# Kernel optimization log

Measured on AMD Instinct MI355X. Metric: run time of the kernel, lower is better.

The kernel has to match this reference:

```python
import jax, jax.numpy as jnp
import numpy as np

DIM = 33  # hardcoded in the torch module


def setup_inputs() -> dict:
    key = jax.random.key(0)
    k1, k2, k3 = jax.random.split(key, 3)
    B, H, W = 8, 512, 512
    inp = jax.random.uniform(k1, (B, 3, H, W), dtype=jnp.float32)
    out = jax.random.uniform(k2, (B, 3, H, W), dtype=jnp.float32)
    mask = (jax.random.uniform(k3, (B, 1, H, W)) > 0.5).astype(jnp.float32)
    return {"mask": mask, "input": inp, "output": out}


def _tridistribute(mask, inp, out, dim=DIM):
    # Trilinear scatter-accumulate of `out` pixel colors into a per-image
    # 3D LUT indexed by `inp` pixel colors, masked, then count-normalized.
    B = inp.shape[0]
    binsize = 1.000001 / (dim - 1)
    x = inp / binsize                              # [B,3,H,W]
    idx = jnp.floor(x).astype(jnp.int32)           # lower bin ids, in [0, dim-2]
    frac = x - jnp.floor(x)                        # trilinear fractions
    r_id, g_id, b_id = idx[:, 0], idx[:, 1], idx[:, 2]
    rd = frac[:, 0].reshape(B, -1)                 # [B,N], N = H*W
    gd = frac[:, 1].reshape(B, -1)
    bd = frac[:, 2].reshape(B, -1)
    base = (r_id + g_id * dim + b_id * dim * dim).reshape(B, -1)  # flat corner 000
    m = (mask[:, 0] > 0).astype(inp.dtype).reshape(B, -1)
    ws, offs = [], []
    for db in (0, 1):
        for dg in (0, 1):
            for dr in (0, 1):
                w = ((rd if dr else 1 - rd) * (gd if dg else 1 - gd) * (bd if db else 1 - bd))
                ws.append(w * m)
                offs.append(dr + dg * dim + db * dim * dim)
    w_all = jnp.stack(ws, 0)                                        # [8,B,N]
    idx_all = base[None] + jnp.asarray(offs, jnp.int32)[:, None, None]  # [8,B,N]
    idx_flat = idx_all.transpose(1, 0, 2).reshape(B, -1)            # [B,8N]
    w_flat = w_all.transpose(1, 0, 2).reshape(B, -1)                # [B,8N]
    out_f = out.reshape(B, 3, -1)                                   # [B,3,N]
    vals = (w_all[:, :, None, :] * out_f[None]).transpose(1, 2, 0, 3).reshape(B, 3, -1)  # [B,3,8N]
    nbins = dim ** 3
    # scatter-add per batch element (vmap over B, then over 3 channels)
    lut = jax.vmap(lambda i, v: jax.vmap(lambda vc: jnp.zeros(nbins, inp.dtype).at[i].add(vc))(v))(idx_flat, vals)  # [B,3,nbins]
    cnt1 = jax.vmap(lambda i, w: jnp.zeros(nbins, inp.dtype).at[i].add(w))(idx_flat, w_flat)  # [B,nbins]
    cnt = jnp.broadcast_to(cnt1[:, None, :], lut.shape)             # same count for all 3 channels
    denom = jnp.where(cnt > 0, cnt, 1.0)
    lut = jnp.where(cnt > 0, lut / denom, 0.0)                      # tridistribute.divide
    shape5 = (B, 3, dim, dim, dim)
    return lut.reshape(shape5), cnt.reshape(shape5)


def reference(mask, input, output):
    lut, lut_count = _tridistribute(mask, input, output)
    return lut, lut_count, output
```

## Files before the change

kernel.cpp:

```cpp
#include <hip/hip_runtime.h>
#include <hip/hip_fp16.h>

#define DIM   33
#define NB    (DIM * DIM * DIM)
#define BATCH 8
#define HW    (512 * 512)
#define SLICE (DIM * DIM)
#define NK1   32
#define CAP1  4416
#define W1    256
#define SPAN1 1024
#define SUB2  4
#define NKEY  1024
#define CAP2  192
#define MAXC2 1120

#define G1_OFF 0
#define G2_OFF 256
#define NCNT   (G2_OFF + BATCH * NKEY)
#define A1     8448
#define S1     (BATCH * NK1 * CAP1)
#define A2     (A1 + 3 * S1)
#define S2     (BATCH * NKEY * CAP2)
#define WS_WORDS (A2 + 3 * S2)

static __device__ __forceinline__ unsigned f2h(float x) {
    return (unsigned)__half_as_ushort(__float2half(x));
}
static __device__ __forceinline__ float h2f(unsigned u) {
    return __half2float(__ushort_as_half((unsigned short)(u & 0xffffu)));
}
static __device__ __forceinline__ unsigned pack2(float a, float b) {
    return f2h(a) | (f2h(b) << 16);
}

__global__ __launch_bounds__(256) void zero_counters(int* __restrict__ ws)
{
    int i = blockIdx.x * 256 + threadIdx.x;
    if (i < NCNT) ws[i] = 0;
}

__global__ __launch_bounds__(256) void sort1(const float* __restrict__ mask,
                                             const float* __restrict__ inp,
                                             const float* __restrict__ outp,
                                             int* __restrict__ ws,
                                             float* __restrict__ outcopy)
{
    __shared__ int hist[NK1], basev[NK1], startL[NK1];
    __shared__ unsigned       stX[SPAN1];
    __shared__ unsigned       stY[SPAN1];
    __shared__ unsigned       o01[SPAN1];
    __shared__ unsigned short o2h[SPAN1];
    __shared__ unsigned short rnk[SPAN1];
    __shared__ unsigned short sidx[SPAN1];

    const int bid = blockIdx.x;
    const int w   = bid & (W1 - 1);
    const int b   = bid >> 8;

    if (threadIdx.x < NK1) hist[threadIdx.x] = 0;
    __syncthreads();

    const float binsize = 1.000001f / 32.0f;
    const size_t off = (size_t)w * SPAN1;
    const float* mk  = mask + (size_t)b * HW + off;
    const float* inR = inp  + (size_t)b * 3 * HW + off;
    const float* inG = inR + HW;
    const float* inB = inR + 2 * HW;
    const float* oR  = outp + (size_t)b * 3 * HW + off;
    const float* oG  = oR + HW;
    const float* oB  = oR + 2 * HW;
    float* cR = outcopy + (size_t)b * 3 * HW + off;
    float* cG = cR + HW;
    float* cB = cR + 2 * HW;

    const int o = threadIdx.x * 4;

    {
        float4 mv = *(const float4*)(mk + o);
        float4 rv = *(const float4*)(inR + o);
        float4 gv = *(const float4*)(inG + o);
        float4 bv = *(const float4*)(inB + o);
        float mm[4] = {mv.x, mv.y, mv.z, mv.w};
        float rr[4] = {rv.x, rv.y, rv.z, rv.w};
        float gg[4] = {gv.x, gv.y, gv.z, gv.w};
        float bb[4] = {bv.x, bv.y, bv.z, bv.w};
        #pragma unroll
        for (int r = 0; r < 4; ++r) {
            unsigned sx = 0, sy = 0;
            if (mm[r] > 0.0f) {
                float xr = rr[r] / binsize;
                float xg = gg[r] / binsize;
                float xb = bb[r] / binsize;
                float fr = floorf(xr), fg = floorf(xg), fb = floorf(xb);
                int ir = (int)fr, ig = (int)fg, ib = (int)fb;
                int rd12 = (int)((xr - fr) * 4095.0f + 0.5f);
                int gd12 = (int)((xg - fg) * 4095.0f + 0.5f);
                int bd12 = (int)((xb - fb) * 4095.0f + 0.5f);
                sx = (unsigned)ir | ((unsigned)ig << 5) | ((unsigned)rd12 << 10)
                   | ((unsigned)(gd12 & 0x3FF) << 22);
                sy = (unsigned)(gd12 >> 10) | ((unsigned)bd12 << 2)
                   | ((unsigned)ib << 14) | (1u << 19);
                rnk[o + r] = (unsigned short)atomicAdd(&hist[ib], 1);
            }
            stX[o + r] = sx;
            stY[o + r] = sy;
        }
    }
    __syncthreads();

    if (threadIdx.x < NK1) {
        int c = hist[threadIdx.x];
        basev[threadIdx.x] = c ? atomicAdd(&ws[G1_OFF + b * NK1 + threadIdx.x], c) : 0;
        int v = c;
        #pragma unroll
        for (int d = 1; d < 32; d <<= 1) {
            int t = __shfl_up(v, d);
            if (threadIdx.x >= d) v += t;
        }
        startL[threadIdx.x] = v - c;
    }
    __syncthreads();

    {
        float4 a0 = *(const float4*)(oR + o);
        float4 a1 = *(const float4*)(oG + o);
        float4 a2 = *(const float4*)(oB + o);
        *(float4*)(cR + o) = a0;
        *(float4*)(cG + o) = a1;
        *(float4*)(cB + o) = a2;
        float q0[4] = {a0.x, a0.y, a0.z, a0.w};
        float q1[4] = {a1.x, a1.y, a1.z, a1.w};
        float q2[4] = {a2.x, a2.y, a2.z, a2.w};
        #pragma unroll
        for (int r = 0; r < 4; ++r) {
            o01[o + r] = pack2(q0[r], q1[r]);
            o2h[o + r] = (unsigned short)f2h(q2[r]);
            unsigned sy = stY[o + r];
            if (sy >> 19) {
                int k = (sy >> 14) & 31;
                sidx[startL[k] + rnk[o + r]] = (unsigned short)(o + r);
            }
        }
    }
    __syncthreads();

    const int nlive = startL[NK1 - 1] + hist[NK1 - 1];
    unsigned* x1 = (unsigned*)(ws + A1);
    unsigned* y1 = x1 + S1;
    unsigned* z1 = x1 + 2 * S1;
    for (int j = threadIdx.x; j < nlive; j += 256) {
        int t = sidx[j];
        unsigned sy = stY[t];
        int k = (sy >> 14) & 31;
        int gs = basev[k] + (j - startL[k]);
        if (gs < CAP1) {
            size_t base = (size_t)(b * NK1 + k) * CAP1 + gs;
            x1[base] = stX[t];
            y1[base] = (sy & 0x3FFFu) | ((o01[t] & 0xFFFFu) << 14);
            z1[base] = (o01[t] >> 16) | ((unsigned)o2h[t] << 16);
        }
    }
}

__global__ __launch_bounds__(256) void sort2(int* __restrict__ ws)
{
    __shared__ unsigned       xL[MAXC2], yL[MAXC2], zL[MAXC2];
    __shared__ unsigned short rnkL[MAXC2], sidxL[MAXC2];
    __shared__ int hist[32], basev[32], startL[32];

    const int bid = blockIdx.x;
    const int s   = bid & (SUB2 - 1);
    const int ib  = (bid >> 2) & 31;
    const int b   = bid >> 7;

    if (threadIdx.x < 32) hist[threadIdx.x] = 0;
    __syncthreads();

    int n1 = ws[G1_OFF + b * NK1 + ib];
    if (n1 > CAP1) n1 = CAP1;
    const int beg = n1 * s / SUB2;
    const int end = n1 * (s + 1) / SUB2;
    const int cntn = end - beg;

    const unsigned* x1 = (const unsigned*)(ws + A1);
    const unsigned* y1 = x1 + S1;
    const unsigned* z1 = x1 + 2 * S1;
    const size_t base1 = (size_t)(b * NK1 + ib) * CAP1 + beg;

    for (int i = threadIdx.x; i < cntn; i += 256) {
        unsigned x = x1[base1 + i];
        xL[i] = x;
        yL[i] = y1[base1 + i];
        zL[i] = z1[base1 + i];
        rnkL[i] = (unsigned short)atomicAdd(&hist[(x >> 5) & 31], 1);
    }
    __syncthreads();

    if (threadIdx.x < 32) {
        int c = hist[threadIdx.x];
        basev[threadIdx.x] = c
            ? atomicAdd(&ws[G2_OFF + ((b << 10) | (threadIdx.x << 5) | ib)], c) : 0;
        int v = c;
        #pragma unroll
        for (int d = 1; d < 32; d <<= 1) {
            int t = __shfl_up(v, d);
            if (threadIdx.x >= d) v += t;
        }
        startL[threadIdx.x] = v - c;
    }
    __syncthreads();

    for (int i = threadIdx.x; i < cntn; i += 256) {
        int k = (xL[i] >> 5) & 31;
        sidxL[startL[k] + rnkL[i]] = (unsigned short)i;
    }
    __syncthreads();

    unsigned* x2 = (unsigned*)(ws + A2);
    unsigned* y2 = x2 + S2;
    unsigned* z2 = x2 + 2 * S2;
    for (int j = threadIdx.x; j < cntn; j += 256) {
        int t = sidxL[j];
        unsigned x = xL[t];
        int k = (x >> 5) & 31;
        int gs = basev[k] + (j - startL[k]);
        if (gs < CAP2) {
            size_t b2 = (size_t)((b << 10) | (k << 5) | ib) * CAP2 + gs;
            x2[b2] = x;
            y2[b2] = yL[t];
            z2[b2] = zL[t];
        }
    }
}

__global__ __launch_bounds__(256) void gather_pass(const int* __restrict__ ws,
                                                   float* __restrict__ lut,
                                                   float* __restrict__ cnt)
{
    __shared__ float4         vL[4][CAP2];
    __shared__ float          rdL[4][CAP2];
    __shared__ unsigned short sidxL[4][CAP2];
    __shared__ int            histL[4][32];
    __shared__ int            startL[4][32];
    __shared__ float          partL[4][DIM][4];

    const int bid   = blockIdx.x;
    const int b     = bid / SLICE;
    const int rem   = bid % SLICE;
    const int gOut  = rem / DIM;
    const int blOut = rem % DIM;

    const int wv    = threadIdx.x >> 6;
    const int lane  = threadIdx.x & 63;
    const int ghalf = (wv >> 1) & 1;
    const int bhalf = wv & 1;
    const int ig    = gOut - 1 + ghalf;
    const int ib    = blOut - 1 + bhalf;
    const bool valid = ((unsigned)ig < 32u) && ((unsigned)ib < 32u);

    if (lane < 32) histL[wv][lane] = 0;
    __syncthreads();

    const unsigned* x2 = (const unsigned*)(ws + A2);
    const unsigned* y2 = x2 + S2;
    const unsigned* z2 = x2 + 2 * S2;

    const float inv = 1.0f / 4095.0f;
    int n = 0;
    int ranks[3] = {0, 0, 0};
    int irs[3]   = {0, 0, 0};
    if (valid) {
        int key = (ig << 5) | ib;
        n = ws[G2_OFF + ((b << 10) | key)];
        if (n > CAP2) n = CAP2;
        size_t kb = (size_t)((b << 10) | key) * CAP2;
        #pragma unroll
        for (int t = 0; t < 3; ++t) {
            int i = lane + t * 64;
            if (i < n) {
                unsigned x = x2[kb + i];
                unsigned y = y2[kb + i];
                unsigned z = z2[kb + i];
                float rd = (float)((x >> 10) & 0xFFF) * inv;
                float gd = (float)(((x >> 22) & 0x3FF) | ((y & 3u) << 10)) * inv;
                float bd = (float)((y >> 2) & 0xFFF) * inv;
                float o0 = h2f(y >> 14);
                float o1 = h2f(z);
                float o2 = h2f(z >> 16);
                float wg_ = ghalf ? (1.0f - gd) : gd;
                float wb_ = bhalf ? (1.0f - bd) : bd;
                float wgb = wg_ * wb_;
                vL[wv][i] = make_float4(wgb, wgb * o0, wgb * o1, wgb * o2);
                rdL[wv][i] = rd;
                irs[t] = x & 31;
                ranks[t] = atomicAdd(&histL[wv][irs[t]], 1);
            }
        }
    }
    __syncthreads();

    {
        int h = (lane < 32) ? histL[wv][lane] : 0;
        int v = h;
        #pragma unroll
        for (int o = 1; o < 32; o <<= 1) {
            int t = __shfl_up(v, o, 32);
            if ((lane & 31) >= o) v += t;
        }
        if (lane < 32) startL[wv][lane] = v - h;
    }
    __syncthreads();

    if (valid) {
        #pragma unroll
        for (int t = 0; t < 3; ++t) {
            int i = lane + t * 64;
            if (i < n)
                sidxL[wv][startL[wv][irs[t]] + ranks[t]] = (unsigned short)i;
        }
    }
    __syncthreads();

    float a0 = 0.f, a1 = 0.f, a2 = 0.f, a3 = 0.f;
    if (valid && lane < DIM) {
        #pragma unroll
        for (int k = 0; k < 2; ++k) {
            int run = lane - 1 + k;
            if ((unsigned)run < 32u) {
                int s = startL[wv][run];
                int e = s + histL[wv][run];
                for (int j = s; j < e; ++j) {
                    int t = sidxL[wv][j];
                    float rd = rdL[wv][t];
                    float4 v = vL[wv][t];
                    float wr_ = k ? (1.0f - rd) : rd;
                    a3 += wr_ * v.x;
                    a0 += wr_ * v.y;
                    a1 += wr_ * v.z;
                    a2 += wr_ * v.w;
                }
            }
        }
    }
    if (lane < DIM) {
        partL[wv][lane][0] = a0;
        partL[wv][lane][1] = a1;
        partL[wv][lane][2] = a2;
        partL[wv][lane][3] = a3;
    }
    __syncthreads();

    if (threadIdx.x < DIM * 4) {
        int r  = threadIdx.x >> 2;
        int ch = threadIdx.x & 3;
        float v = partL[0][r][ch] + partL[1][r][ch] + partL[2][r][ch] + partL[3][r][ch];
        float c = partL[0][r][3]  + partL[1][r][3]  + partL[2][r][3]  + partL[3][r][3];
        int bin = r + gOut * DIM + blOut * SLICE;
        size_t ob = (size_t)b * 3 * NB;
        if (ch == 3) {
            cnt[ob + bin]          = c;
            cnt[ob + NB + bin]     = c;
            cnt[ob + 2 * NB + bin] = c;
        } else {
            lut[ob + (size_t)ch * NB + bin] = (c > 0.0f) ? v / c : 0.0f;
        }
    }
}

__global__ void tridist_scatter(const float* __restrict__ mask,
                                const float* __restrict__ inp,
                                const float* __restrict__ outp,
                                float* __restrict__ lut,
                                float* __restrict__ cnt)
{
    int i = blockIdx.x * blockDim.x + threadIdx.x;
    if (i >= BATCH * HW) return;
    int b = i / HW;
    int p = i - b * HW;

    float m = mask[(size_t)b * HW + p];
    if (!(m > 0.0f)) return;

    const float binsize = 1.000001f / 32.0f;
    size_t ibase = (size_t)b * 3 * HW + p;
    float xr = inp[ibase] / binsize;
    float xg = inp[ibase + HW] / binsize;
    float xb = inp[ibase + 2 * HW] / binsize;
    float flr = floorf(xr), flg = floorf(xg), flb = floorf(xb);
    int ir = (int)flr, ig = (int)flg, ib = (int)flb;
    float rd = xr - flr, gd = xg - flg, bd = xb - flb;
    int base = ir + ig * DIM + ib * DIM * DIM;
    float o0 = outp[ibase], o1 = outp[ibase + HW], o2 = outp[ibase + 2 * HW];
    float wr[2] = {1.0f - rd, rd};
    float wg_[2] = {1.0f - gd, gd};
    float wb[2] = {1.0f - bd, bd};
    float* lut0 = lut + (size_t)b * 3 * NB;
    float* cnt0 = cnt + (size_t)b * 3 * NB;
    #pragma unroll
    for (int db = 0; db < 2; ++db)
        #pragma unroll
        for (int dg = 0; dg < 2; ++dg)
            #pragma unroll
            for (int dr = 0; dr < 2; ++dr) {
                float wv2 = (wr[dr] * wg_[dg]) * wb[db];
                int bin = base + dr + dg * DIM + db * DIM * DIM;
                atomicAdd(cnt0 + bin, wv2);
                atomicAdd(lut0 + bin, wv2 * o0);
                atomicAdd(lut0 + NB + bin, wv2 * o1);
                atomicAdd(lut0 + 2 * NB + bin, wv2 * o2);
            }
}

__global__ void tridist_finalize(float* __restrict__ lut, float* __restrict__ cnt)
{
    int i = blockIdx.x * blockDim.x + threadIdx.x;
    if (i >= BATCH * NB) return;
    int b = i / NB;
    int j = i - b * NB;
    float c = cnt[(size_t)b * 3 * NB + j];
    bool nz = (c > 0.0f);
    #pragma unroll
    for (int ch = 0; ch < 3; ++ch) {
        size_t off = ((size_t)b * 3 + ch) * NB + j;
        float v = lut[off];
        lut[off] = nz ? (v / c) : 0.0f;
        cnt[off] = c;
    }
}

__global__ void copy_out(const float4* __restrict__ src,
                         float4* __restrict__ dst, int n4)
{
    int i = blockIdx.x * blockDim.x + threadIdx.x;
    int stride = gridDim.x * blockDim.x;
    for (; i < n4; i += stride) dst[i] = src[i];
}

extern "C" void kernel_launch(void* const* d_in, const int* in_sizes, int n_in,
                              void* d_out, int out_size, void* d_ws, size_t ws_size,
                              hipStream_t stream)
{
    const float* mask = (const float*)d_in[0];
    const float* inp  = (const float*)d_in[1];
    const float* outp = (const float*)d_in[2];

    float* out     = (float*)d_out;
    float* lut     = out;
    float* cnt     = out + (size_t)BATCH * 3 * NB;
    float* outcopy = out + (size_t)2 * BATCH * 3 * NB;

    size_t need = (size_t)WS_WORDS * sizeof(int);

    if (ws_size >= need) {
        int* ws = (int*)d_ws;
        zero_counters<<<(NCNT + 255) / 256, 256, 0, stream>>>(ws);
        sort1<<<BATCH * W1, 256, 0, stream>>>(mask, inp, outp, ws, outcopy);
        sort2<<<BATCH * NK1 * SUB2, 256, 0, stream>>>(ws);
        gather_pass<<<BATCH * SLICE, 256, 0, stream>>>(ws, lut, cnt);
    } else {
        hipMemsetAsync(out, 0, (size_t)2 * BATCH * 3 * NB * sizeof(float), stream);
        tridist_scatter<<<(BATCH * HW + 255) / 256, 256, 0, stream>>>(mask, inp, outp, lut, cnt);
        tridist_finalize<<<(BATCH * NB + 255) / 256, 256, 0, stream>>>(lut, cnt);
        int n4 = BATCH * 3 * HW / 4;
        copy_out<<<2048, 256, 0, stream>>>((const float4*)outp, (float4*)outcopy, n4);
    }
}
```

Baseline: 69.05 us.

## Split gather accumulation across 64 lanes with precomputed per-corner weighted values

In the gather pass, each point now stores two precomputed float4 values (weights times colors for both r-corners), and every lane of the wave accumulates one (run, corner) pair, so all 64 lanes work instead of 33, each doing two serial run loops. The final reduction combines the per-lane partials from adjacent runs. In the first kernel, the output-colour loads, copy and half-packing move into the first phase, next to the input loads. This doubles the shared-memory footprint of the value buffers and adds a little reduction logic.

```diff
diff --git a/kernel.cpp b/kernel.cpp
--- a/kernel.cpp
+++ b/kernel.cpp
@@ -81,12 +81,25 @@
         float4 rv = *(const float4*)(inR + o);
         float4 gv = *(const float4*)(inG + o);
         float4 bv = *(const float4*)(inB + o);
+        float4 a0 = *(const float4*)(oR + o);
+        float4 a1 = *(const float4*)(oG + o);
+        float4 a2 = *(const float4*)(oB + o);
+
+        *(float4*)(cR + o) = a0;
+        *(float4*)(cG + o) = a1;
+        *(float4*)(cB + o) = a2;
+
         float mm[4] = {mv.x, mv.y, mv.z, mv.w};
         float rr[4] = {rv.x, rv.y, rv.z, rv.w};
         float gg[4] = {gv.x, gv.y, gv.z, gv.w};
         float bb[4] = {bv.x, bv.y, bv.z, bv.w};
+        float q0[4] = {a0.x, a0.y, a0.z, a0.w};
+        float q1[4] = {a1.x, a1.y, a1.z, a1.w};
+        float q2[4] = {a2.x, a2.y, a2.z, a2.w};
         #pragma unroll
         for (int r = 0; r < 4; ++r) {
+            o01[o + r] = pack2(q0[r], q1[r]);
+            o2h[o + r] = (unsigned short)f2h(q2[r]);
             unsigned sx = 0, sy = 0;
             if (mm[r] > 0.0f) {
                 float xr = rr[r] / binsize;
@@ -123,19 +136,8 @@
     __syncthreads();
 
     {
-        float4 a0 = *(const float4*)(oR + o);
-        float4 a1 = *(const float4*)(oG + o);
-        float4 a2 = *(const float4*)(oB + o);
-        *(float4*)(cR + o) = a0;
-        *(float4*)(cG + o) = a1;
-        *(float4*)(cB + o) = a2;
-        float q0[4] = {a0.x, a0.y, a0.z, a0.w};
-        float q1[4] = {a1.x, a1.y, a1.z, a1.w};
-        float q2[4] = {a2.x, a2.y, a2.z, a2.w};
         #pragma unroll
         for (int r = 0; r < 4; ++r) {
-            o01[o + r] = pack2(q0[r], q1[r]);
-            o2h[o + r] = (unsigned short)f2h(q2[r]);
             unsigned sy = stY[o + r];
             if (sy >> 19) {
                 int k = (sy >> 14) & 31;
@@ -238,12 +240,11 @@
                                                    float* __restrict__ lut,
                                                    float* __restrict__ cnt)
 {
-    __shared__ float4         vL[4][CAP2];
-    __shared__ float          rdL[4][CAP2];
+    __shared__ float4         vK[4][2][CAP2];
     __shared__ unsigned short sidxL[4][CAP2];
     __shared__ int            histL[4][32];
     __shared__ int            startL[4][32];
-    __shared__ float          partL[4][DIM][4];
+    __shared__ float          partL[4][64][4];
 
     const int bid   = blockIdx.x;
     const int b     = bid / SLICE;
@@ -291,8 +292,10 @@
                 float wg_ = ghalf ? (1.0f - gd) : gd;
                 float wb_ = bhalf ? (1.0f - bd) : bd;
                 float wgb = wg_ * wb_;
-                vL[wv][i] = make_float4(wgb, wgb * o0, wgb * o1, wgb * o2);
-                rdL[wv][i] = rd;
+                float w0 = wgb * rd;
+                float w1 = wgb * (1.0f - rd);
+                vK[wv][0][i] = make_float4(w0 * o0, w0 * o1, w0 * o2, w0);
+                vK[wv][1][i] = make_float4(w1 * o0, w1 * o1, w1 * o2, w1);
                 irs[t] = x & 31;
                 ranks[t] = atomicAdd(&histL[wv][irs[t]], 1);
             }
@@ -322,40 +325,35 @@
     }
     __syncthreads();
 
-    float a0 = 0.f, a1 = 0.f, a2 = 0.f, a3 = 0.f;
-    if (valid && lane < DIM) {
-        #pragma unroll
-        for (int k = 0; k < 2; ++k) {
-            int run = lane - 1 + k;
-            if ((unsigned)run < 32u) {
-                int s = startL[wv][run];
-                int e = s + histL[wv][run];
-                for (int j = s; j < e; ++j) {
-                    int t = sidxL[wv][j];
-                    float rd = rdL[wv][t];
-                    float4 v = vL[wv][t];
-                    float wr_ = k ? (1.0f - rd) : rd;
-                    a3 += wr_ * v.x;
-                    a0 += wr_ * v.y;
-                    a1 += wr_ * v.z;
-                    a2 += wr_ * v.w;
-                }
-            }
-        }
-    }
-    if (lane < DIM) {
-        partL[wv][lane][0] = a0;
-        partL[wv][lane][1] = a1;
-        partL[wv][lane][2] = a2;
-        partL[wv][lane][3] = a3;
-    }
+    float4 acc = make_float4(0.f, 0.f, 0.f, 0.f);
+    if (valid) {
+        const int run = lane >> 1;
+        const int kk  = lane & 1;
+        int s = startL[wv][run];
+        int e = s + histL[wv][run];
+        for (int j = s; j < e; ++j) {
+            float4 v = vK[wv][kk][sidxL[wv][j]];
+            acc.x += v.x; acc.y += v.y; acc.z += v.z; acc.w += v.w;
+        }
+    }
+    *(float4*)partL[wv][lane] = acc;
     __syncthreads();
 
     if (threadIdx.x < DIM * 4) {
         int r  = threadIdx.x >> 2;
         int ch = threadIdx.x & 3;
-        float v = partL[0][r][ch] + partL[1][r][ch] + partL[2][r][ch] + partL[3][r][ch];
-        float c = partL[0][r][3]  + partL[1][r][3]  + partL[2][r][3]  + partL[3][r][3];
+        float v = 0.f, c = 0.f;
+        #pragma unroll
+        for (int w2 = 0; w2 < 4; ++w2) {
+            if (r < 32) {
+                v += partL[w2][2 * r + 1][ch == 3 ? 3 : ch];
+                c += partL[w2][2 * r + 1][3];
+            }
+            if (r > 0) {
+                v += partL[w2][2 * r - 2][ch == 3 ? 3 : ch];
+                c += partL[w2][2 * r - 2][3];
+            }
+        }
         int bin = r + gOut * DIM + blOut * SLICE;
         size_t ob = (size_t)b * 3 * NB;
         if (ch == 3) {
```

Measured after the change: 71.65 us. 3.8% more time.
